# Kernel optimization log

Measured on AMD Instinct MI355X. Metric: run time of the kernel, lower is better.

Reference implementation:

```python
import jax, jax.numpy as jnp
import numpy as np

N_TOKENS = 65536
D_MODEL = 256
D_HID = 256
N_EXPERTS = 8


def setup_inputs() -> dict:
    key = jax.random.key(0)
    ks = jax.random.split(key, 6)
    x = jax.random.normal(ks[0], (N_TOKENS, D_MODEL), dtype=jnp.float32)
    # gate Linear weight [E, d] (torch Linear stores [out, in]); small init like nn.Linear default scale
    wg = jax.random.normal(ks[1], (N_EXPERTS, D_MODEL), dtype=jnp.float32) * 0.06
    W1 = jax.random.normal(ks[2], (N_EXPERTS, D_MODEL, D_HID), dtype=jnp.float32) * 0.06
    b1 = jnp.zeros((N_EXPERTS, D_HID), dtype=jnp.float32)
    W2 = jax.random.normal(ks[3], (N_EXPERTS, D_HID, D_MODEL), dtype=jnp.float32) * 0.06
    b2 = jnp.zeros((N_EXPERTS, D_MODEL), dtype=jnp.float32)
    return {"x": x, "wg": wg, "W1": W1, "b1": b1, "W2": W2, "b2": b2}


def reference(x, wg, W1, b1, W2, b2):
    # Gate: logits = x @ wg.T ; softmax over experts ; top-1 gate value + assignment
    gates = jax.nn.softmax(x @ wg.T, axis=1)                  # [N, E]
    gate_val = jnp.max(gates, axis=1)                          # [N] == topk(k=1) values
    assign = jnp.argmax(gates, axis=1)                         # [N] expert id per token

    out = jnp.zeros_like(x)
    # Fixed small loop over experts (structural, not data-dim); each iter is one dense GEMM pair.
    for e in range(N_EXPERTS):
        h = jax.nn.relu(x @ W1[e] + b1[e])                     # [N, D_HID]
        y_e = h @ W2[e] + b2[e]                                # [N, D_MODEL]
        sel = (assign == e)[:, None]
        out = jnp.where(sel, y_e * gate_val[:, None], out)
    return out
```

## Files before the change

kernel.cpp:

```cpp
#include <hip/hip_runtime.h>
#include <hip/hip_bf16.h>
#include <math.h>

#define NTOK 65536
#define DMODEL 256
#define NEXP 8
#define CAP 65536
#define MAXTILES 1040
#define CSTRIDE 64

typedef __bf16 bf16_t;
typedef __bf16 bf16x8 __attribute__((ext_vector_type(8)));
typedef float f32x4 __attribute__((ext_vector_type(4)));

__device__ inline void async16(const void* g, void* l) {
  __builtin_amdgcn_global_load_lds(
      (const __attribute__((address_space(1))) unsigned int*)g,
      (__attribute__((address_space(3))) unsigned int*)l, 16, 0, 0);
}

__global__ void prep_kernel(const float* __restrict__ wg, float* __restrict__ wgT,
                            int* __restrict__ counts) {
  int t = blockIdx.x * 256 + threadIdx.x;
  if (t < NEXP * DMODEL) wgT[t] = wg[(t & 7) * 256 + (t >> 3)];
  if (t < NEXP * CSTRIDE) counts[t] = 0;
}

__global__ __launch_bounds__(256) void castT_kernel(
    const float* __restrict__ W1, const float* __restrict__ W2,
    bf16_t* __restrict__ w1t, bf16_t* __restrict__ w2t) {
  __shared__ float tile[32][33];
  const int m = blockIdx.z;
  const float* src = (m < 8) ? (W1 + (size_t)m * 65536) : (W2 + (size_t)(m - 8) * 65536);
  bf16_t* dst = (m < 8) ? (w1t + (size_t)m * 65536) : (w2t + (size_t)(m - 8) * 65536);
  const int x0 = blockIdx.x * 32, y0 = blockIdx.y * 32;
  const int tx = threadIdx.x, ty = threadIdx.y;
#pragma unroll
  for (int i = 0; i < 4; ++i)
    tile[ty + i * 8][tx] = src[(size_t)(y0 + ty + i * 8) * 256 + x0 + tx];
  __syncthreads();
#pragma unroll
  for (int i = 0; i < 4; ++i)
    dst[(size_t)(x0 + ty + i * 8) * 256 + y0 + tx] = (bf16_t)tile[tx][ty + i * 8];
}

__global__ __launch_bounds__(256) void gate_kernel(
    const float* __restrict__ x, const float* __restrict__ wgT,
    bf16_t* __restrict__ xb, float* __restrict__ gateval,
    int* __restrict__ counts, int* __restrict__ idxbuf) {
  __shared__ __align__(16) float xs[64 * 256];
  __shared__ double part[3][64][9];
  const int th = threadIdx.x;
  const int lane = th & 63;
  const int wv = th >> 6;
  const int tokbase = blockIdx.x * 64;

#pragma unroll
  for (int i = 0; i < 16; ++i) {
    int p = i * 256 + th;
    int r = p >> 6;
    int c = (p & 63) ^ (r & 31);
    async16(x + (size_t)(tokbase + r) * 256 + c * 4,
            &xs[(i * 256 + wv * 64) * 4]);
  }
  __syncthreads();

#pragma unroll
  for (int i = 0; i < 8; ++i) {
    int p = i * 256 + th;
    int r = p >> 5, cb = p & 31;
    int mk = r & 31;
    f32x4 a = *(const f32x4*)&xs[r * 256 + (((2 * cb) ^ mk) * 4)];
    f32x4 b = *(const f32x4*)&xs[r * 256 + (((2 * cb + 1) ^ mk) * 4)];
    bf16x8 bv;
    bv[0] = (bf16_t)a[0]; bv[1] = (bf16_t)a[1];
    bv[2] = (bf16_t)a[2]; bv[3] = (bf16_t)a[3];
    bv[4] = (bf16_t)b[0]; bv[5] = (bf16_t)b[1];
    bv[6] = (bf16_t)b[2]; bv[7] = (bf16_t)b[3];
    *(bf16x8*)(xb + (size_t)tokbase * 256 + (size_t)p * 8) = bv;
  }

  const float* wp = wgT + wv * 64 * 8;
  const int xm = lane & 31;
  double acc[8] = {0, 0, 0, 0, 0, 0, 0, 0};
#pragma unroll
  for (int u = 0; u < 8; ++u) {
    int c0 = 16 * wv + 2 * u;
    f32x4 a = *(const f32x4*)&xs[lane * 256 + ((c0 ^ xm) * 4)];
    f32x4 b = *(const f32x4*)&xs[lane * 256 + (((c0 + 1) ^ xm) * 4)];
    float xv[8] = {a[0], a[1], a[2], a[3], b[0], b[1], b[2], b[3]};
    float s[8] = {0.f, 0.f, 0.f, 0.f, 0.f, 0.f, 0.f, 0.f};
#pragma unroll
    for (int j = 0; j < 8; ++j) {
      f32x4 w0 = *(const f32x4*)&wp[(u * 8 + j) * 8];
      f32x4 w1 = *(const f32x4*)&wp[(u * 8 + j) * 8 + 4];
      s[0] = fmaf(xv[j], w0[0], s[0]); s[1] = fmaf(xv[j], w0[1], s[1]);
      s[2] = fmaf(xv[j], w0[2], s[2]); s[3] = fmaf(xv[j], w0[3], s[3]);
      s[4] = fmaf(xv[j], w1[0], s[4]); s[5] = fmaf(xv[j], w1[1], s[5]);
      s[6] = fmaf(xv[j], w1[2], s[6]); s[7] = fmaf(xv[j], w1[3], s[7]);
    }
#pragma unroll
    for (int e = 0; e < 8; ++e) acc[e] += (double)s[e];
  }

  if (wv > 0) {
#pragma unroll
    for (int e = 0; e < 8; ++e) part[wv - 1][lane][e] = acc[e];
  }
  __syncthreads();
  if (wv == 0) {
#pragma unroll
    for (int s2 = 0; s2 < 3; ++s2)
#pragma unroll
      for (int e = 0; e < 8; ++e) acc[e] += part[s2][lane][e];
    double m = acc[0]; int bi = 0;
#pragma unroll
    for (int e = 1; e < 8; ++e) if (acc[e] > m) { m = acc[e]; bi = e; }
    float denom = 0.f;
#pragma unroll
    for (int e = 0; e < 8; ++e) denom += __expf((float)(acc[e] - m));
    const int tok = tokbase + lane;
    gateval[tok] = 1.0f / denom;
    unsigned long long mymask = 0;
#pragma unroll
    for (int e = 0; e < NEXP; ++e) {
      unsigned long long mk = __ballot(bi == e);
      if (lane == e) mymask = mk;
    }
    int mybase = 0;
    if (lane < NEXP) mybase = atomicAdd(&counts[lane * CSTRIDE], (int)__popcll(mymask));
#pragma unroll
    for (int e = 0; e < NEXP; ++e) {
      unsigned long long mk = __ballot(bi == e);
      int b = __shfl(mybase, e, 64);
      if (bi == e) {
        int pos = b + (int)__popcll(mk & ((1ull << lane) - 1ull));
        idxbuf[e * CAP + pos] = tok;
      }
    }
  }
}

__global__ void scan_kernel(const int* __restrict__ counts, int* __restrict__ bases,
                            int* __restrict__ tl, int* __restrict__ ntiles) {
  int t = threadIdx.x;
  if (t == 0) {
    int s = 0, n = 0;
    for (int e = 0; e < NEXP; ++e) {
      bases[e] = s; s += counts[e * CSTRIDE];
      n += (counts[e * CSTRIDE] + 63) >> 6;
    }
    *ntiles = n;
  }
  if (t < NEXP) {
    int off = 0;
    for (int j = 0; j < t; ++j) off += (counts[j * CSTRIDE] + 63) >> 6;
    int n = (counts[t * CSTRIDE] + 63) >> 6;
    for (int k = 0; k < n; ++k) tl[off + k] = t | (k << 3);
  }
}

__global__ __launch_bounds__(512, 4) void moe_gemm_kernel(
    const bf16_t* __restrict__ xb, const bf16_t* __restrict__ w1t,
    const bf16_t* __restrict__ w2t, const float* __restrict__ b1,
    const float* __restrict__ b2, const float* __restrict__ gateval,
    const int* __restrict__ counts, const int* __restrict__ bases,
    const int* __restrict__ idxbuf, const int* __restrict__ tl,
    const int* __restrict__ ntiles, float* __restrict__ out) {
  if ((int)blockIdx.x >= *ntiles) return;
  const int tle = tl[blockIdx.x];
  const int e = tle & 7, tm = tle >> 3;
  const int cnt = counts[e * CSTRIDE];
  (void)bases;
  __shared__ __align__(16) bf16_t ts[64 * 256];
  __shared__ int sidx[64];
  __shared__ float sgv[64];
  const int th = threadIdx.x;
  const int lane = th & 63, wv = th >> 6;
  const int lr = lane & 15, lq = lane >> 4;
  if (th < 64) {
    int r = tm * 64 + th;
    int t = idxbuf[e * CAP + (r < cnt ? r : cnt - 1)];
    sidx[th] = t;
    sgv[th] = gateval[t];
  }
  __syncthreads();
#pragma unroll
  for (int i = 0; i < 4; ++i) {
    int p = i * 512 + th;
    int r = p >> 5, s = (p & 31) ^ (r & 31);
    async16(xb + (size_t)sidx[r] * 256 + s * 8, &ts[(i * 512 + wv * 64) * 8]);
  }
  __syncthreads();

  const bf16_t* w1e = w1t + (size_t)e * 65536;
  {
    f32x4 acc[4][2] = {};
#pragma unroll
    for (int kk = 0; kk < 256; kk += 64) {
#pragma unroll
      for (int kb = 0; kb < 2; ++kb) {
        const int ks = (kk >> 3) + kb * 4 + lq;
        bf16x8 af[4], bfr[2];
#pragma unroll
        for (int mi = 0; mi < 4; ++mi) {
          int r = mi * 16 + lr;
          af[mi] = *(const bf16x8*)&ts[(r * 32 + (ks ^ (r & 31))) * 8];
        }
#pragma unroll
        for (int ni = 0; ni < 2; ++ni) {
          int n = wv * 32 + ni * 16 + lr;
          bfr[ni] = *(const bf16x8*)&w1e[(size_t)n * 256 + kk + kb * 32 + lq * 8];
        }
#pragma unroll
        for (int mi = 0; mi < 4; ++mi)
#pragma unroll
          for (int ni = 0; ni < 2; ++ni)
            acc[mi][ni] = __builtin_amdgcn_mfma_f32_16x16x32_bf16(af[mi], bfr[ni], acc[mi][ni], 0, 0, 0);
      }
    }
    float b1v[2];
#pragma unroll
    for (int ni = 0; ni < 2; ++ni) b1v[ni] = b1[e * 256 + wv * 32 + ni * 16 + lr];
    __syncthreads();
#pragma unroll
    for (int mi = 0; mi < 4; ++mi)
#pragma unroll
      for (int ni = 0; ni < 2; ++ni)
#pragma unroll
        for (int rr = 0; rr < 4; ++rr) {
          int m = mi * 16 + lq * 4 + rr;
          int n = wv * 32 + ni * 16 + lr;
          float v = acc[mi][ni][rr] + b1v[ni];
          v = v > 0.f ? v : 0.f;
          ts[(m * 32 + ((n >> 3) ^ (m & 31))) * 8 + (n & 7)] = (bf16_t)v;
        }
  }
  __syncthreads();

  const bf16_t* w2e = w2t + (size_t)e * 65536;
  {
    f32x4 acc[4][2] = {};
#pragma unroll
    for (int kk = 0; kk < 256; kk += 64) {
#pragma unroll
      for (int kb = 0; kb < 2; ++kb) {
        const int ks = (kk >> 3) + kb * 4 + lq;
        bf16x8 af[4], bfr[2];
#pragma unroll
        for (int mi = 0; mi < 4; ++mi) {
          int r = mi * 16 + lr;
          af[mi] = *(const bf16x8*)&ts[(r * 32 + (ks ^ (r & 31))) * 8];
        }
#pragma unroll
        for (int ni = 0; ni < 2; ++ni) {
          int n = wv * 32 + ni * 16 + lr;
          bfr[ni] = *(const bf16x8*)&w2e[(size_t)n * 256 + kk + kb * 32 + lq * 8];
        }
#pragma unroll
        for (int mi = 0; mi < 4; ++mi)
#pragma unroll
          for (int ni = 0; ni < 2; ++ni)
            acc[mi][ni] = __builtin_amdgcn_mfma_f32_16x16x32_bf16(af[mi], bfr[ni], acc[mi][ni], 0, 0, 0);
      }
    }
    float b2v[2];
#pragma unroll
    for (int ni = 0; ni < 2; ++ni) b2v[ni] = b2[e * 256 + wv * 32 + ni * 16 + lr];
#pragma unroll
    for (int mi = 0; mi < 4; ++mi)
#pragma unroll
      for (int rr = 0; rr < 4; ++rr) {
        int m = mi * 16 + lq * 4 + rr;
        int row = tm * 64 + m;
        if (row < cnt) {
          int tok = sidx[m];
          float g = sgv[m];
#pragma unroll
          for (int ni = 0; ni < 2; ++ni) {
            int n = wv * 32 + ni * 16 + lr;
            out[(size_t)tok * 256 + n] = (acc[mi][ni][rr] + b2v[ni]) * g;
          }
        }
      }
  }
}

extern "C" void kernel_launch(void* const* d_in, const int* in_sizes, int n_in,
                              void* d_out, int out_size, void* d_ws, size_t ws_size,
                              hipStream_t stream) {
  (void)in_sizes; (void)n_in; (void)out_size; (void)ws_size;
  const float* x  = (const float*)d_in[0];
  const float* wg = (const float*)d_in[1];
  const float* W1 = (const float*)d_in[2];
  const float* b1 = (const float*)d_in[3];
  const float* W2 = (const float*)d_in[4];
  const float* b2 = (const float*)d_in[5];
  float* out = (float*)d_out;

  char* ws = (char*)d_ws;
  size_t off = 0;
  auto alloc = [&](size_t bytes) {
    void* p = ws + off;
    off += (bytes + 255) & ~(size_t)255;
    return p;
  };
  bf16_t* xb     = (bf16_t*)alloc((size_t)NTOK * DMODEL * 2);
  bf16_t* w1t    = (bf16_t*)alloc((size_t)NEXP * 256 * 256 * 2);
  bf16_t* w2t    = (bf16_t*)alloc((size_t)NEXP * 256 * 256 * 2);
  int*    idxbuf = (int*)alloc((size_t)NEXP * CAP * 4);
  float*  gv     = (float*)alloc((size_t)NTOK * 4);
  float*  wgT    = (float*)alloc((size_t)NEXP * DMODEL * 4);
  int*    tilel  = (int*)alloc((size_t)MAXTILES * 4);
  int*    counts = (int*)alloc((size_t)NEXP * CSTRIDE * 4);
  int*    bases  = (int*)alloc(64);
  int*    ntiles = (int*)alloc(64);

  hipLaunchKernelGGL(prep_kernel, dim3(8), dim3(256), 0, stream, wg, wgT, counts);
  hipLaunchKernelGGL(castT_kernel, dim3(8, 8, 16), dim3(32, 8), 0, stream, W1, W2, w1t, w2t);
  hipLaunchKernelGGL(gate_kernel, dim3(NTOK / 64), dim3(256), 0, stream,
                     x, wgT, xb, gv, counts, idxbuf);
  hipLaunchKernelGGL(scan_kernel, dim3(1), dim3(64), 0, stream, counts, bases, tilel, ntiles);
  hipLaunchKernelGGL(moe_gemm_kernel, dim3(MAXTILES), dim3(512), 0, stream,
                     xb, w1t, w2t, b1, b2, gv, counts, bases, idxbuf, tilel, ntiles, out);
}
```

Baseline: 200.0 us.

## Fuse weight packing into gate kernel and compute tile map inside GEMM

Removes the prep, transpose-cast and scan kernels. The gate kernel now also packs W1/W2 into an MFMA-fragment-ready bf16 layout, two fragments per block, and reads wg directly. It stages x through a half-sized LDS buffer in two halves, which may raise occupancy. The GEMM kernel derives its expert and tile index from the counts inline, and B-fragment loads become contiguous per-lane 16-byte reads. The aim is to cut launch overhead and non-coalesced weight loads, at the cost of an extra LDS sync round in the gate kernel and scattered 2-byte stores during packing.

```diff
diff --git a/kernel.cpp b/kernel.cpp
--- a/kernel.cpp
+++ b/kernel.cpp
@@ -19,88 +19,83 @@
       (__attribute__((address_space(3))) unsigned int*)l, 16, 0, 0);
 }
 
-__global__ void prep_kernel(const float* __restrict__ wg, float* __restrict__ wgT,
-                            int* __restrict__ counts) {
-  int t = blockIdx.x * 256 + threadIdx.x;
-  if (t < NEXP * DMODEL) wgT[t] = wg[(t & 7) * 256 + (t >> 3)];
-  if (t < NEXP * CSTRIDE) counts[t] = 0;
-}
-
-__global__ __launch_bounds__(256) void castT_kernel(
+__global__ __launch_bounds__(256) void gate_pack_kernel(
+    const float* __restrict__ x, const float* __restrict__ wg,
     const float* __restrict__ W1, const float* __restrict__ W2,
-    bf16_t* __restrict__ w1t, bf16_t* __restrict__ w2t) {
-  __shared__ float tile[32][33];
-  const int m = blockIdx.z;
-  const float* src = (m < 8) ? (W1 + (size_t)m * 65536) : (W2 + (size_t)(m - 8) * 65536);
-  bf16_t* dst = (m < 8) ? (w1t + (size_t)m * 65536) : (w2t + (size_t)(m - 8) * 65536);
-  const int x0 = blockIdx.x * 32, y0 = blockIdx.y * 32;
-  const int tx = threadIdx.x, ty = threadIdx.y;
-#pragma unroll
-  for (int i = 0; i < 4; ++i)
-    tile[ty + i * 8][tx] = src[(size_t)(y0 + ty + i * 8) * 256 + x0 + tx];
-  __syncthreads();
-#pragma unroll
-  for (int i = 0; i < 4; ++i)
-    dst[(size_t)(x0 + ty + i * 8) * 256 + y0 + tx] = (bf16_t)tile[tx][ty + i * 8];
-}
-
-__global__ __launch_bounds__(256) void gate_kernel(
-    const float* __restrict__ x, const float* __restrict__ wgT,
     bf16_t* __restrict__ xb, float* __restrict__ gateval,
-    int* __restrict__ counts, int* __restrict__ idxbuf) {
-  __shared__ __align__(16) float xs[64 * 256];
+    int* __restrict__ counts, int* __restrict__ idxbuf,
+    bf16_t* __restrict__ w1p, bf16_t* __restrict__ w2p) {
+  __shared__ __align__(16) float xs[64 * 128];
   __shared__ double part[3][64][9];
   const int th = threadIdx.x;
   const int lane = th & 63;
   const int wv = th >> 6;
   const int tokbase = blockIdx.x * 64;
-
-#pragma unroll
-  for (int i = 0; i < 16; ++i) {
-    int p = i * 256 + th;
-    int r = p >> 6;
-    int c = (p & 63) ^ (r & 31);
-    async16(x + (size_t)(tokbase + r) * 256 + c * 4,
-            &xs[(i * 256 + wv * 64) * 4]);
-  }
-  __syncthreads();
+  const int xm = lane & 31;
+  double acc[8] = {0, 0, 0, 0, 0, 0, 0, 0};
 
 #pragma unroll
   for (int i = 0; i < 8; ++i) {
     int p = i * 256 + th;
-    int r = p >> 5, cb = p & 31;
-    int mk = r & 31;
-    f32x4 a = *(const f32x4*)&xs[r * 256 + (((2 * cb) ^ mk) * 4)];
-    f32x4 b = *(const f32x4*)&xs[r * 256 + (((2 * cb + 1) ^ mk) * 4)];
-    bf16x8 bv;
-    bv[0] = (bf16_t)a[0]; bv[1] = (bf16_t)a[1];
-    bv[2] = (bf16_t)a[2]; bv[3] = (bf16_t)a[3];
-    bv[4] = (bf16_t)b[0]; bv[5] = (bf16_t)b[1];
-    bv[6] = (bf16_t)b[2]; bv[7] = (bf16_t)b[3];
-    *(bf16x8*)(xb + (size_t)tokbase * 256 + (size_t)p * 8) = bv;
-  }
-
-  const float* wp = wgT + wv * 64 * 8;
-  const int xm = lane & 31;
-  double acc[8] = {0, 0, 0, 0, 0, 0, 0, 0};
-#pragma unroll
-  for (int u = 0; u < 8; ++u) {
-    int c0 = 16 * wv + 2 * u;
-    f32x4 a = *(const f32x4*)&xs[lane * 256 + ((c0 ^ xm) * 4)];
-    f32x4 b = *(const f32x4*)&xs[lane * 256 + (((c0 + 1) ^ xm) * 4)];
-    float xv[8] = {a[0], a[1], a[2], a[3], b[0], b[1], b[2], b[3]};
-    float s[8] = {0.f, 0.f, 0.f, 0.f, 0.f, 0.f, 0.f, 0.f};
-#pragma unroll
-    for (int j = 0; j < 8; ++j) {
-      f32x4 w0 = *(const f32x4*)&wp[(u * 8 + j) * 8];
-      f32x4 w1 = *(const f32x4*)&wp[(u * 8 + j) * 8 + 4];
-      s[0] = fmaf(xv[j], w0[0], s[0]); s[1] = fmaf(xv[j], w0[1], s[1]);
-      s[2] = fmaf(xv[j], w0[2], s[2]); s[3] = fmaf(xv[j], w0[3], s[3]);
-      s[4] = fmaf(xv[j], w1[0], s[4]); s[5] = fmaf(xv[j], w1[1], s[5]);
-      s[6] = fmaf(xv[j], w1[2], s[6]); s[7] = fmaf(xv[j], w1[3], s[7]);
-    }
-#pragma unroll
-    for (int e = 0; e < 8; ++e) acc[e] += (double)s[e];
+    int r = p >> 5, c = (p & 31) ^ (r & 31);
+    async16(x + (size_t)(tokbase + r) * 256 + c * 4, &xs[(i * 256 + wv * 64) * 4]);
+  }
+#pragma unroll
+  for (int jj = 0; jj < 2; ++jj) {
+    int f = blockIdx.x * 2 + jj;
+    int mat = f >> 10, e = (f >> 7) & 7, kf = (f >> 4) & 7, nt = f & 15;
+    const float* src = (mat == 0 ? W1 : W2) + (size_t)e * 65536;
+    bf16_t* dst = (mat == 0 ? w1p : w2p) + (((size_t)e * 8 + kf) * 16 + nt) * 512;
+#pragma unroll
+    for (int rep = 0; rep < 2; ++rep) {
+      int kl = rep * 16 + (th >> 4), nl = th & 15;
+      float v = src[(size_t)(kf * 32 + kl) * 256 + nt * 16 + nl];
+      int lanep = nl + 16 * (kl >> 3), j = kl & 7;
+      dst[lanep * 8 + j] = (bf16_t)v;
+    }
+  }
+  __syncthreads();
+
+#pragma unroll
+  for (int h = 0; h < 2; ++h) {
+#pragma unroll
+    for (int i = 0; i < 4; ++i) {
+      int p = i * 256 + th;
+      int r = p >> 4, cb = p & 15, mk = r & 31;
+      f32x4 a = *(const f32x4*)&xs[r * 128 + (((2 * cb) ^ mk) * 4)];
+      f32x4 b = *(const f32x4*)&xs[r * 128 + (((2 * cb + 1) ^ mk) * 4)];
+      bf16x8 bv;
+      bv[0] = (bf16_t)a[0]; bv[1] = (bf16_t)a[1];
+      bv[2] = (bf16_t)a[2]; bv[3] = (bf16_t)a[3];
+      bv[4] = (bf16_t)b[0]; bv[5] = (bf16_t)b[1];
+      bv[6] = (bf16_t)b[2]; bv[7] = (bf16_t)b[3];
+      *(bf16x8*)(xb + (size_t)(tokbase + r) * 256 + h * 128 + cb * 8) = bv;
+    }
+#pragma unroll
+    for (int g = 0; g < 4; ++g) {
+      int c0 = wv * 8 + 2 * g;
+      f32x4 a = *(const f32x4*)&xs[lane * 128 + ((c0 ^ xm) * 4)];
+      f32x4 b = *(const f32x4*)&xs[lane * 128 + (((c0 + 1) ^ xm) * 4)];
+      float xv[8] = {a[0], a[1], a[2], a[3], b[0], b[1], b[2], b[3]};
+#pragma unroll
+      for (int e = 0; e < 8; ++e) {
+        const float* wge = wg + e * 256 + h * 128 + wv * 32 + g * 8;
+        float s = 0.f;
+#pragma unroll
+        for (int j2 = 0; j2 < 8; ++j2) s = fmaf(xv[j2], wge[j2], s);
+        acc[e] += (double)s;
+      }
+    }
+    if (h == 0) {
+      __syncthreads();
+#pragma unroll
+      for (int i = 0; i < 8; ++i) {
+        int p = i * 256 + th;
+        int r = p >> 5, c = (p & 31) ^ (r & 31);
+        async16(x + (size_t)(tokbase + r) * 256 + 128 + c * 4, &xs[(i * 256 + wv * 64) * 4]);
+      }
+      __syncthreads();
+    }
   }
 
   if (wv > 0) {
@@ -141,37 +136,24 @@
   }
 }
 
-__global__ void scan_kernel(const int* __restrict__ counts, int* __restrict__ bases,
-                            int* __restrict__ tl, int* __restrict__ ntiles) {
-  int t = threadIdx.x;
-  if (t == 0) {
-    int s = 0, n = 0;
-    for (int e = 0; e < NEXP; ++e) {
-      bases[e] = s; s += counts[e * CSTRIDE];
-      n += (counts[e * CSTRIDE] + 63) >> 6;
-    }
-    *ntiles = n;
-  }
-  if (t < NEXP) {
-    int off = 0;
-    for (int j = 0; j < t; ++j) off += (counts[j * CSTRIDE] + 63) >> 6;
-    int n = (counts[t * CSTRIDE] + 63) >> 6;
-    for (int k = 0; k < n; ++k) tl[off + k] = t | (k << 3);
-  }
-}
-
 __global__ __launch_bounds__(512, 4) void moe_gemm_kernel(
-    const bf16_t* __restrict__ xb, const bf16_t* __restrict__ w1t,
-    const bf16_t* __restrict__ w2t, const float* __restrict__ b1,
+    const bf16_t* __restrict__ xb, const bf16_t* __restrict__ w1p,
+    const bf16_t* __restrict__ w2p, const float* __restrict__ b1,
     const float* __restrict__ b2, const float* __restrict__ gateval,
-    const int* __restrict__ counts, const int* __restrict__ bases,
-    const int* __restrict__ idxbuf, const int* __restrict__ tl,
-    const int* __restrict__ ntiles, float* __restrict__ out) {
-  if ((int)blockIdx.x >= *ntiles) return;
-  const int tle = tl[blockIdx.x];
-  const int e = tle & 7, tm = tle >> 3;
-  const int cnt = counts[e * CSTRIDE];
-  (void)bases;
+    const int* __restrict__ counts, const int* __restrict__ idxbuf,
+    float* __restrict__ out) {
+  int ex = -1, tm = 0, a2 = 0, cnte = 0;
+#pragma unroll
+  for (int e2 = 0; e2 < 8; ++e2) {
+    int c = counts[e2 * CSTRIDE];
+    int n = (c + 63) >> 6;
+    if ((int)blockIdx.x >= a2 && (int)blockIdx.x < a2 + n) {
+      ex = e2; tm = (int)blockIdx.x - a2; cnte = c;
+    }
+    a2 += n;
+  }
+  if (ex < 0) return;
+  const int ccnt = cnte;
   __shared__ __align__(16) bf16_t ts[64 * 256];
   __shared__ int sidx[64];
   __shared__ float sgv[64];
@@ -180,7 +162,7 @@
   const int lr = lane & 15, lq = lane >> 4;
   if (th < 64) {
     int r = tm * 64 + th;
-    int t = idxbuf[e * CAP + (r < cnt ? r : cnt - 1)];
+    int t = idxbuf[ex * CAP + (r < ccnt ? r : ccnt - 1)];
     sidx[th] = t;
     sgv[th] = gateval[t];
   }
@@ -193,7 +175,7 @@
   }
   __syncthreads();
 
-  const bf16_t* w1e = w1t + (size_t)e * 65536;
+  const bf16_t* w1e = w1p + (size_t)ex * 65536;
   {
     f32x4 acc[4][2] = {};
 #pragma unroll
@@ -201,6 +183,7 @@
 #pragma unroll
       for (int kb = 0; kb < 2; ++kb) {
         const int ks = (kk >> 3) + kb * 4 + lq;
+        const int kf = (kk >> 5) + kb;
         bf16x8 af[4], bfr[2];
 #pragma unroll
         for (int mi = 0; mi < 4; ++mi) {
@@ -208,10 +191,8 @@
           af[mi] = *(const bf16x8*)&ts[(r * 32 + (ks ^ (r & 31))) * 8];
         }
 #pragma unroll
-        for (int ni = 0; ni < 2; ++ni) {
-          int n = wv * 32 + ni * 16 + lr;
-          bfr[ni] = *(const bf16x8*)&w1e[(size_t)n * 256 + kk + kb * 32 + lq * 8];
-        }
+        for (int ni = 0; ni < 2; ++ni)
+          bfr[ni] = *(const bf16x8*)&w1e[((size_t)kf * 16 + wv * 2 + ni) * 512 + lane * 8];
 #pragma unroll
         for (int mi = 0; mi < 4; ++mi)
 #pragma unroll
@@ -221,7 +202,7 @@
     }
     float b1v[2];
 #pragma unroll
-    for (int ni = 0; ni < 2; ++ni) b1v[ni] = b1[e * 256 + wv * 32 + ni * 16 + lr];
+    for (int ni = 0; ni < 2; ++ni) b1v[ni] = b1[ex * 256 + wv * 32 + ni * 16 + lr];
     __syncthreads();
 #pragma unroll
     for (int mi = 0; mi < 4; ++mi)
@@ -238,7 +219,7 @@
   }
   __syncthreads();
 
-  const bf16_t* w2e = w2t + (size_t)e * 65536;
+  const bf16_t* w2e = w2p + (size_t)ex * 65536;
   {
     f32x4 acc[4][2] = {};
 #pragma unroll
@@ -246,6 +227,7 @@
 #pragma unroll
       for (int kb = 0; kb < 2; ++kb) {
         const int ks = (kk >> 3) + kb * 4 + lq;
+        const int kf = (kk >> 5) + kb;
         bf16x8 af[4], bfr[2];
 #pragma unroll
         for (int mi = 0; mi < 4; ++mi) {
@@ -253,10 +235,8 @@
           af[mi] = *(const bf16x8*)&ts[(r * 32 + (ks ^ (r & 31))) * 8];
         }
 #pragma unroll
-        for (int ni = 0; ni < 2; ++ni) {
-          int n = wv * 32 + ni * 16 + lr;
-          bfr[ni] = *(const bf16x8*)&w2e[(size_t)n * 256 + kk + kb * 32 + lq * 8];
-        }
+        for (int ni = 0; ni < 2; ++ni)
+          bfr[ni] = *(const bf16x8*)&w2e[((size_t)kf * 16 + wv * 2 + ni) * 512 + lane * 8];
 #pragma unroll
         for (int mi = 0; mi < 4; ++mi)
 #pragma unroll
@@ -266,20 +246,20 @@
     }
     float b2v[2];
 #pragma unroll
-    for (int ni = 0; ni < 2; ++ni) b2v[ni] = b2[e * 256 + wv * 32 + ni * 16 + lr];
+    for (int ni = 0; ni < 2; ++ni) b2v[ni] = b2[ex * 256 + wv * 32 + ni * 16 + lr];
 #pragma unroll
     for (int mi = 0; mi < 4; ++mi)
 #pragma unroll
       for (int rr = 0; rr < 4; ++rr) {
         int m = mi * 16 + lq * 4 + rr;
         int row = tm * 64 + m;
-        if (row < cnt) {
-          int tok = sidx[m];
+        if (row < ccnt) {
+          int tk = sidx[m];
           float g = sgv[m];
 #pragma unroll
           for (int ni = 0; ni < 2; ++ni) {
             int n = wv * 32 + ni * 16 + lr;
-            out[(size_t)tok * 256 + n] = (acc[mi][ni][rr] + b2v[ni]) * g;
+            out[(size_t)tk * 256 + n] = (acc[mi][ni][rr] + b2v[ni]) * g;
           }
         }
       }
@@ -306,21 +286,15 @@
     return p;
   };
   bf16_t* xb     = (bf16_t*)alloc((size_t)NTOK * DMODEL * 2);
-  bf16_t* w1t    = (bf16_t*)alloc((size_t)NEXP * 256 * 256 * 2);
-  bf16_t* w2t    = (bf16_t*)alloc((size_t)NEXP * 256 * 256 * 2);
+  bf16_t* w1p    = (bf16_t*)alloc((size_t)NEXP * 256 * 256 * 2);
+  bf16_t* w2p    = (bf16_t*)alloc((size_t)NEXP * 256 * 256 * 2);
   int*    idxbuf = (int*)alloc((size_t)NEXP * CAP * 4);
   float*  gv     = (float*)alloc((size_t)NTOK * 4);
-  float*  wgT    = (float*)alloc((size_t)NEXP * DMODEL * 4);
-  int*    tilel  = (int*)alloc((size_t)MAXTILES * 4);
   int*    counts = (int*)alloc((size_t)NEXP * CSTRIDE * 4);
-  int*    bases  = (int*)alloc(64);
-  int*    ntiles = (int*)alloc(64);
-
-  hipLaunchKernelGGL(prep_kernel, dim3(8), dim3(256), 0, stream, wg, wgT, counts);
-  hipLaunchKernelGGL(castT_kernel, dim3(8, 8, 16), dim3(32, 8), 0, stream, W1, W2, w1t, w2t);
-  hipLaunchKernelGGL(gate_kernel, dim3(NTOK / 64), dim3(256), 0, stream,
-                     x, wgT, xb, gv, counts, idxbuf);
-  hipLaunchKernelGGL(scan_kernel, dim3(1), dim3(64), 0, stream, counts, bases, tilel, ntiles);
+
+  hipMemsetAsync(counts, 0, (size_t)NEXP * CSTRIDE * 4, stream);
+  hipLaunchKernelGGL(gate_pack_kernel, dim3(NTOK / 64), dim3(256), 0, stream,
+                     x, wg, W1, W2, xb, gv, counts, idxbuf, w1p, w2p);
   hipLaunchKernelGGL(moe_gemm_kernel, dim3(MAXTILES), dim3(512), 0, stream,
-                     xb, w1t, w2t, b1, b2, gv, counts, bases, idxbuf, tilel, ntiles, out);
+                     xb, w1p, w2p, b1, b2, gv, counts, idxbuf, out);
 }
```

New measurement: 173.3 us. 13.4% less time.
